# Optimization experiments

Hardware: AMD Instinct MI355X
Metric: run time of the kernel (lower is better)

## Reference

```python
import jax, jax.numpy as jnp
import numpy as np
from jax import lax

HEADS = 8
PS = 4  # window size


def setup_inputs() -> dict:
    key = jax.random.key(0)
    k1, k2, k3, k4 = jax.random.split(key, 4)
    b, c, h, w = 8, 256, 128, 128
    x = jax.random.normal(k1, (b, c, h, w), dtype=jnp.float32)
    W_qkv = jax.random.normal(k2, (3 * c, c), dtype=jnp.float32) * 0.05
    W_dw = jax.random.normal(k3, (3 * c, 1, 3, 3), dtype=jnp.float32) * 0.1
    temperature = jnp.ones((HEADS, 1, 1), dtype=jnp.float32)
    W_proj = jax.random.normal(k4, (c, c), dtype=jnp.float32) * 0.05
    return {"x": x, "W_qkv": W_qkv, "W_dw": W_dw, "temperature": temperature, "W_proj": W_proj}


def _l2norm(t, eps=1e-12):
    # matches torch F.normalize(dim=-1): x / max(||x||_2, eps)
    n = jnp.sqrt(jnp.sum(t * t, axis=-1, keepdims=True))
    return t / jnp.maximum(n, eps)


def reference(x, W_qkv, W_dw, temperature, W_proj):
    b, c, h0, w0 = x.shape
    ps, heads = PS, HEADS
    pad_h = (ps - h0 % ps) % ps
    pad_w = (ps - w0 % ps) % ps
    if pad_h or pad_w:
        x = jnp.pad(x, ((0, 0), (0, 0), (0, pad_h), (0, pad_w)))
    H, W = x.shape[2], x.shape[3]
    nh, nw = H // ps, W // ps
    d = c // heads

    # 1x1 conv -> depthwise 3x3 conv (groups = 3c, padding 1)
    qkv = jnp.einsum('oc,bchw->bohw', W_qkv, x)
    qkv = lax.conv_general_dilated(qkv, W_dw, (1, 1), 'SAME',
                                   feature_group_count=3 * c,
                                   dimension_numbers=('NCHW', 'OIHW', 'NCHW'))
    q, k, v = jnp.split(qkv, 3, axis=1)

    def win(t):
        # b (head d) (nh ps) (nw ps) -> b (nh nw) head d (ps ps)
        t = t.reshape(b, heads, d, nh, ps, nw, ps)
        t = t.transpose(0, 3, 5, 1, 2, 4, 6)  # b nh nw head d ps ps
        return t.reshape(b, nh * nw, heads, d, ps * ps)

    q, k, v = win(q), win(k), win(v)
    q = _l2norm(q)
    k = _l2norm(k)

    # channel attention over head-dim d, keys/queries live in the ps*ps window
    attn = jnp.einsum('bnhde,bnhfe->bnhdf', q, k) * temperature  # (b,n,head,d,d)
    attn = jax.nn.softmax(attn, axis=-1)
    out = jnp.einsum('bnhdf,bnhfe->bnhde', attn, v)  # (b,n,head,d,ps*ps)

    # inverse rearrange -> b (head d) H W
    out = out.reshape(b, nh, nw, heads, d, ps, ps)
    out = out.transpose(0, 3, 4, 1, 5, 2, 6).reshape(b, c, H, W)
    out = jnp.einsum('oc,bchw->bohw', W_proj, out)
    if pad_h or pad_w:
        out = out[:, :, :h0, :w0]
    return out
```

## Files before the change

kernel.cpp:

```cpp
#include <hip/hip_runtime.h>
#include <math.h>


#define HW_ (128*128)
#define CHW_ (256*128*128)

typedef __attribute__((ext_vector_type(8))) short short8;
typedef __attribute__((ext_vector_type(4))) short shortv4;
typedef __attribute__((ext_vector_type(4))) float f32x4;

static __device__ __forceinline__ unsigned short f2bf(float f) {
    unsigned int u = __float_as_uint(f);
    unsigned int r = (u + 0x7fffu + ((u >> 16) & 1u)) >> 16;
    return (unsigned short)r;
}
static __device__ __forceinline__ float bf2f(unsigned short u) {
    return __uint_as_float(((unsigned int)u) << 16);
}

__global__ __launch_bounds__(256) void conv_w(
    const float* __restrict__ Wq, const float* __restrict__ Wp,
    unsigned short* __restrict__ out)
{
    int i = blockIdx.x * 256 + threadIdx.x;
    float v = (i < 196608) ? Wq[i] : Wp[i - 196608];
    out[i] = f2bf(v);
}

__global__ __launch_bounds__(256) void gemm_qkv(
    const unsigned short* __restrict__ A,
    const float* __restrict__ x,
    unsigned short* __restrict__ qkv)
{
    __shared__ __align__(16) char smem[16896];
    shortv4* Bq = (shortv4*)(smem + 8192);

    const int t = threadIdx.x;
    const int lane = t & 63, wid = t >> 6;
    const int m0 = blockIdx.x * 128;
    const int by = blockIdx.y;
    const int nb = by >> 7;
    const int nloc0 = (by & 127) * 128;
    const int wr = wid >> 1, wc = wid & 1;
    const int l15 = lane & 15, l4 = lane >> 4;

    const unsigned short* srcA[2];
    #pragma unroll
    for (int i = 0; i < 2; ++i) {
        int u = i * 256 + t;
        int r = u >> 2, cs = u & 3;
        int c = cs ^ ((r ^ (r >> 2)) & 3);
        srcA[i] = A + (size_t)(m0 + r) * 256 + c * 8;
    }
    int ar[4];
    #pragma unroll
    for (int i = 0; i < 4; ++i) {
        int rm = wr * 64 + i * 16 + l15;
        ar[i] = rm * 4 + (l4 ^ ((rm ^ (rm >> 2)) & 3));
    }

    const int tp = t & 127, th = t >> 7;
    const float* xb = x + (size_t)nb * CHW_ + nloc0 + tp;

    f32x4 acc[4][4];
    #pragma unroll
    for (int i = 0; i < 4; ++i)
        #pragma unroll
        for (int j = 0; j < 4; ++j)
            acc[i][j] = (f32x4){0.f, 0.f, 0.f, 0.f};

    const short8* Ab = (const short8*)smem;

    for (int k0 = 0; k0 < 256; k0 += 32) {
        __syncthreads();
        float bv[16];
        #pragma unroll
        for (int j = 0; j < 4; ++j)
            #pragma unroll
            for (int i = 0; i < 4; ++i)
                bv[j * 4 + i] = xb[(size_t)(k0 + th * 16 + j * 4 + i) * HW_];
        #pragma unroll
        for (int i = 0; i < 2; ++i)
            __builtin_amdgcn_global_load_lds(
                (const __attribute__((address_space(1))) void*)(srcA[i] + k0),
                (__attribute__((address_space(3))) void*)(smem + i * 4096 + wid * 1024),
                16, 0, 0);
        #pragma unroll
        for (int j = 0; j < 4; ++j) {
            shortv4 s;
            s.x = (short)f2bf(bv[j * 4 + 0]);
            s.y = (short)f2bf(bv[j * 4 + 1]);
            s.z = (short)f2bf(bv[j * 4 + 2]);
            s.w = (short)f2bf(bv[j * 4 + 3]);
            Bq[(th * 4 + j) * 128 + tp] = s;
        }
        __syncthreads();

        short8 af[4], bf[4];
        #pragma unroll
        for (int i = 0; i < 4; ++i) {
            af[i] = Ab[ar[i]];
            int rn = wc * 64 + i * 16 + l15;
            shortv4 lo = Bq[(l4 * 2) * 128 + rn];
            shortv4 hi = Bq[(l4 * 2 + 1) * 128 + rn];
            short8 b;
            b[0] = lo.x; b[1] = lo.y; b[2] = lo.z; b[3] = lo.w;
            b[4] = hi.x; b[5] = hi.y; b[6] = hi.z; b[7] = hi.w;
            bf[i] = b;
        }
        #pragma unroll
        for (int am = 0; am < 4; ++am)
            #pragma unroll
            for (int bn = 0; bn < 4; ++bn)
                acc[am][bn] = __builtin_amdgcn_mfma_f32_16x16x32_bf16(
                    af[am], bf[bn], acc[am][bn], 0, 0, 0);
    }

    unsigned short* Co = qkv + (size_t)nb * (768 * (size_t)HW_) + nloc0;
    float* ep = (float*)smem;
    const int rr = t >> 3, c0 = (t & 7) * 16;
    #pragma unroll
    for (int am = 0; am < 4; ++am) {
        __syncthreads();
        #pragma unroll
        for (int q = 0; q < 4; ++q)
            #pragma unroll
            for (int bn = 0; bn < 4; ++bn)
                ep[(wr * 16 + l4 * 4 + q) * 132 + wc * 64 + bn * 16 + l15] =
                    acc[am][bn][q];
        __syncthreads();
        short8 o0, o1;
        #pragma unroll
        for (int j = 0; j < 8; ++j) {
            o0[j] = (short)f2bf(ep[rr * 132 + c0 + j]);
            o1[j] = (short)f2bf(ep[rr * 132 + c0 + 8 + j]);
        }
        int m = m0 + (rr >> 4) * 64 + am * 16 + (rr & 15);
        unsigned short* p = Co + (size_t)m * 16384 + c0;
        *reinterpret_cast<short8*>(p) = o0;
        *reinterpret_cast<short8*>(p + 8) = o1;
    }
}

template<int BF16OUT>
__global__ __launch_bounds__(256) void gemm_bf16(
    const unsigned short* __restrict__ A,
    const unsigned short* __restrict__ Bt,
    void* __restrict__ Cv,
    size_t strideBatch)
{
    __shared__ __align__(16) char smem[BF16OUT ? 16896 : 16384];

    const int t = threadIdx.x;
    const int lane = t & 63, wid = t >> 6;
    const int m0 = blockIdx.y * 128, n0 = blockIdx.x * 128;
    const int nb = n0 >> 14, nloc0 = n0 & 16383;
    const int wr = wid >> 1, wc = wid & 1;
    const int l15 = lane & 15, l4 = lane >> 4;

    const unsigned short* srcA[2];
    const unsigned short* srcB[2];
    #pragma unroll
    for (int i = 0; i < 2; ++i) {
        int u = i * 256 + t;
        int r = u >> 2, cs = u & 3;
        int c = cs ^ ((r ^ (r >> 2)) & 3);
        srcA[i] = A  + (size_t)(m0 + r) * 256 + c * 8;
        srcB[i] = Bt + (size_t)(n0 + r) * 256 + c * 8;
    }

    int ar[4], br[4];
    #pragma unroll
    for (int i = 0; i < 4; ++i) {
        int rm = wr * 64 + i * 16 + l15;
        ar[i] = rm * 4 + (l4 ^ ((rm ^ (rm >> 2)) & 3));
        int rn = wc * 64 + i * 16 + l15;
        br[i] = rn * 4 + (l4 ^ ((rn ^ (rn >> 2)) & 3));
    }

    f32x4 acc[4][4];
    #pragma unroll
    for (int i = 0; i < 4; ++i)
        #pragma unroll
        for (int j = 0; j < 4; ++j)
            acc[i][j] = (f32x4){0.f, 0.f, 0.f, 0.f};

    const short8* Ab = (const short8*)smem;
    const short8* Bb = (const short8*)(smem + 8192);

    for (int k0 = 0; k0 < 256; k0 += 32) {
        __syncthreads();
        #pragma unroll
        for (int i = 0; i < 2; ++i) {
            __builtin_amdgcn_global_load_lds(
                (const __attribute__((address_space(1))) void*)(srcA[i] + k0),
                (__attribute__((address_space(3))) void*)(smem + i * 4096 + wid * 1024),
                16, 0, 0);
            __builtin_amdgcn_global_load_lds(
                (const __attribute__((address_space(1))) void*)(srcB[i] + k0),
                (__attribute__((address_space(3))) void*)(smem + 8192 + i * 4096 + wid * 1024),
                16, 0, 0);
        }
        __syncthreads();
        short8 af[4], bf[4];
        #pragma unroll
        for (int i = 0; i < 4; ++i) { af[i] = Ab[ar[i]]; bf[i] = Bb[br[i]]; }
        #pragma unroll
        for (int am = 0; am < 4; ++am)
            #pragma unroll
            for (int bn = 0; bn < 4; ++bn)
                acc[am][bn] = __builtin_amdgcn_mfma_f32_16x16x32_bf16(
                    af[am], bf[bn], acc[am][bn], 0, 0, 0);
    }

    if (BF16OUT) {
        unsigned short* Co = (unsigned short*)Cv + (size_t)nb * strideBatch + nloc0;
        float* ep = (float*)smem;
        const int rr = t >> 3, c0 = (t & 7) * 16;
        #pragma unroll
        for (int am = 0; am < 4; ++am) {
            __syncthreads();
            #pragma unroll
            for (int q = 0; q < 4; ++q)
                #pragma unroll
                for (int bn = 0; bn < 4; ++bn)
                    ep[(wr * 16 + l4 * 4 + q) * 132 + wc * 64 + bn * 16 + l15] =
                        acc[am][bn][q];
            __syncthreads();
            short8 o0, o1;
            #pragma unroll
            for (int j = 0; j < 8; ++j) {
                o0[j] = (short)f2bf(ep[rr * 132 + c0 + j]);
                o1[j] = (short)f2bf(ep[rr * 132 + c0 + 8 + j]);
            }
            int m = m0 + (rr >> 4) * 64 + am * 16 + (rr & 15);
            unsigned short* p = Co + (size_t)m * 16384 + c0;
            *reinterpret_cast<short8*>(p) = o0;
            *reinterpret_cast<short8*>(p + 8) = o1;
        }
    } else {
        float* Co = (float*)Cv + (size_t)nb * strideBatch + nloc0;
        #pragma unroll
        for (int am = 0; am < 4; ++am)
            #pragma unroll
            for (int q = 0; q < 4; ++q) {
                int m = m0 + wr * 64 + am * 16 + l4 * 4 + q;
                #pragma unroll
                for (int bn = 0; bn < 4; ++bn)
                    Co[(size_t)m * 16384 + wc * 64 + bn * 16 + l15] =
                        acc[am][bn][q];
            }
    }
}

__global__ __launch_bounds__(256) void dwconv_win(
    const unsigned short* __restrict__ qkv,
    const float* __restrict__ Wdw,
    unsigned short* __restrict__ dww)
{
    const int t    = threadIdx.x;
    const int lane = t & 63;
    const int iw   = t & 31;
    const int chl  = t >> 5;
    const int wyl  = blockIdx.x;
    const int ch   = blockIdx.y * 8 + chl;
    const int bz   = blockIdx.z;

    float w[9];
    #pragma unroll
    for (int i = 0; i < 9; ++i) w[i] = Wdw[ch * 9 + i];

    float h[6][6];
    const unsigned short* plane = qkv + (size_t)(bz * 768 + ch) * HW_;
    #pragma unroll
    for (int r = 0; r < 6; ++r) {
        int gy = wyl * 4 - 1 + r;
        float c0 = 0.f, c1 = 0.f, c2 = 0.f, c3 = 0.f;
        if (gy >= 0 && gy < 128) {
            ushort4 u = *reinterpret_cast<const ushort4*>(
                plane + (size_t)gy * 128 + iw * 4);
            c0 = bf2f(u.x); c1 = bf2f(u.y); c2 = bf2f(u.z); c3 = bf2f(u.w);
        }
        float lf = __shfl(c3, (lane + 63) & 63);
        float rt = __shfl(c0, (lane + 1) & 63);
        h[r][0] = (iw == 0)  ? 0.f : lf;
        h[r][1] = c0; h[r][2] = c1; h[r][3] = c2; h[r][4] = c3;
        h[r][5] = (iw == 31) ? 0.f : rt;
    }

    unsigned short* outp =
        dww + ((size_t)(bz * 1024 + wyl * 32 + iw) * 768 + ch) * 16;
    short8 o0, o1;
    #pragma unroll
    for (int py = 0; py < 4; ++py) {
        #pragma unroll
        for (int px = 0; px < 4; ++px) {
            float s = 0.f;
            #pragma unroll
            for (int dy = 0; dy < 3; ++dy)
                #pragma unroll
                for (int dx = 0; dx < 3; ++dx)
                    s += h[py + dy][px + dx] * w[dy * 3 + dx];
            int e = py * 4 + px;
            if (e < 8) o0[e] = (short)f2bf(s); else o1[e - 8] = (short)f2bf(s);
        }
    }
    *reinterpret_cast<short8*>(outp) = o0;
    *reinterpret_cast<short8*>(outp + 8) = o1;
}

__global__ __launch_bounds__(256) void attn2(
    const unsigned short* __restrict__ dww,
    const float* __restrict__ temp,
    unsigned short* __restrict__ attnT)
{
    __shared__ float kv[512 * 20];
    const int t   = threadIdx.x;
    const int iw  = blockIdx.x;
    const int wyl = blockIdx.y;
    const int bz  = blockIdx.z;
    const int win = bz * 1024 + wyl * 32 + iw;
    const unsigned short* src = dww + (size_t)win * 12288;

    float q[16], kr[16], vr[16];
    {
        short8 a0 = *reinterpret_cast<const short8*>(src + t * 16);
        short8 a1 = *reinterpret_cast<const short8*>(src + t * 16 + 8);
        short8 b0 = *reinterpret_cast<const short8*>(src + (256 + t) * 16);
        short8 b1 = *reinterpret_cast<const short8*>(src + (256 + t) * 16 + 8);
        short8 c0 = *reinterpret_cast<const short8*>(src + (512 + t) * 16);
        short8 c1 = *reinterpret_cast<const short8*>(src + (512 + t) * 16 + 8);
        #pragma unroll
        for (int j = 0; j < 8; ++j) {
            q[j]      = bf2f((unsigned short)a0[j]);
            q[8 + j]  = bf2f((unsigned short)a1[j]);
            kr[j]     = bf2f((unsigned short)b0[j]);
            kr[8 + j] = bf2f((unsigned short)b1[j]);
            vr[j]     = bf2f((unsigned short)c0[j]);
            vr[8 + j] = bf2f((unsigned short)c1[j]);
        }
    }

    {
        float sq = 0.f, sk = 0.f;
        #pragma unroll
        for (int e = 0; e < 16; ++e) { sq += q[e] * q[e]; sk += kr[e] * kr[e]; }
        float cq = 1.0f / fmaxf(sqrtf(sq), 1e-12f);
        float ck = 1.0f / fmaxf(sqrtf(sk), 1e-12f);
        #pragma unroll
        for (int e = 0; e < 16; ++e) { q[e] *= cq; kr[e] *= ck; }
    }

    {
        float* kp = &kv[t * 20];
        float* vp = &kv[(256 + t) * 20];
        #pragma unroll
        for (int j = 0; j < 4; ++j) {
            *reinterpret_cast<float4*>(kp + j * 4) =
                make_float4(kr[j*4], kr[j*4+1], kr[j*4+2], kr[j*4+3]);
            *reinterpret_cast<float4*>(vp + j * 4) =
                make_float4(vr[j*4], vr[j*4+1], vr[j*4+2], vr[j*4+3]);
        }
    }
    __syncthreads();

    const int head = t >> 5;
    const float tmpv = temp[head];
    const float* kb = &kv[(head * 32) * 20];
    const float* vb = &kv[(256 + head * 32) * 20];

    float lg[32];
    float mx = -1e30f;
    #pragma unroll
    for (int f = 0; f < 32; ++f) {
        float s = 0.f;
        #pragma unroll
        for (int j = 0; j < 4; ++j) {
            float4 k4 = *reinterpret_cast<const float4*>(kb + f * 20 + j * 4);
            s += q[j*4] * k4.x + q[j*4+1] * k4.y + q[j*4+2] * k4.z + q[j*4+3] * k4.w;
        }
        s *= tmpv;
        lg[f] = s;
        mx = fmaxf(mx, s);
    }
    float sum = 0.f;
    #pragma unroll
    for (int f = 0; f < 32; ++f) { lg[f] = __expf(lg[f] - mx); sum += lg[f]; }
    const float inv = 1.0f / sum;

    float o[16];
    #pragma unroll
    for (int e = 0; e < 16; ++e) o[e] = 0.f;
    #pragma unroll
    for (int f = 0; f < 32; ++f) {
        float p = lg[f];
        #pragma unroll
        for (int j = 0; j < 4; ++j) {
            float4 v4 = *reinterpret_cast<const float4*>(vb + f * 20 + j * 4);
            o[j*4]   += p * v4.x; o[j*4+1] += p * v4.y;
            o[j*4+2] += p * v4.z; o[j*4+3] += p * v4.w;
        }
    }

    #pragma unroll
    for (int e = 0; e < 16; ++e) {
        int py = e >> 2, px = e & 3;
        size_t pl = (size_t)bz * HW_ + (wyl * 4 + py) * 128 + iw * 4 + px;
        attnT[pl * 256 + t] = f2bf(o[e] * inv);
    }
}

extern "C" void kernel_launch(void* const* d_in, const int* in_sizes, int n_in,
                              void* d_out, int out_size, void* d_ws, size_t ws_size,
                              hipStream_t stream) {
    const float* x     = (const float*)d_in[0];
    const float* Wqkv  = (const float*)d_in[1];
    const float* Wdw   = (const float*)d_in[2];
    const float* temp  = (const float*)d_in[3];
    const float* Wproj = (const float*)d_in[4];
    float* out = (float*)d_out;

    unsigned short* Wb = (unsigned short*)d_ws;
    const size_t offW = 262144 * 2;

    const size_t qkvB = (size_t)768 * HW_ * 2;
    const size_t dwwB = (size_t)1024 * 768 * 16 * 2;
    const size_t atB  = (size_t)HW_ * 256 * 2;
    const size_t perB = qkvB + dwwB + atB;

    int G = 4;
    while (G > 1 && offW + (size_t)G * perB > ws_size) G >>= 1;

    unsigned short* qkv   = (unsigned short*)((char*)d_ws + offW);
    unsigned short* dww   = (unsigned short*)((char*)d_ws + offW + (size_t)G * qkvB);
    unsigned short* attnT = (unsigned short*)((char*)d_ws + offW + (size_t)G * (qkvB + dwwB));

    conv_w<<<1024, 256, 0, stream>>>(Wqkv, Wproj, Wb);

    for (int b0 = 0; b0 < 8; b0 += G) {
        gemm_qkv<<<dim3(6, G * 128), 256, 0, stream>>>(
            Wb, x + (size_t)b0 * CHW_, qkv);

        dwconv_win<<<dim3(32, 96, G), 256, 0, stream>>>(
            qkv, Wdw, dww);

        attn2<<<dim3(32, 32, G), 256, 0, stream>>>(
            dww, temp, attnT);

        gemm_bf16<0><<<dim3(G * 128, 2), 256, 0, stream>>>(
            Wb + 196608, attnT, out + (size_t)b0 * CHW_, (size_t)CHW_);
    }
}
```

Baseline: 410.3 us.

## Vectorize x loads in QKV GEMM, swap proj grid order, raise batch group

The QKV GEMM now loads x with float4 reads (four pixels per thread across four channels) and packs the bf16 values into a new padded LDS layout with 16-byte stores, replacing scalar loads and 8-byte stores. The projection GEMM grid is transposed so the two M-blocks sharing one N-tile are adjacent, which improves L2 reuse of the attention tile, and its unused bf16 epilogue is removed. The batch group size G is raised from 4 to 8 when the workspace allows it, which means fewer launches and larger grids but needs more workspace memory.

```diff
diff --git a/kernel.cpp b/kernel.cpp
--- a/kernel.cpp
+++ b/kernel.cpp
@@ -33,8 +33,6 @@
     unsigned short* __restrict__ qkv)
 {
     __shared__ __align__(16) char smem[16896];
-    shortv4* Bq = (shortv4*)(smem + 8192);
-
     const int t = threadIdx.x;
     const int lane = t & 63, wid = t >> 6;
     const int m0 = blockIdx.x * 128;
@@ -59,8 +57,11 @@
         ar[i] = rm * 4 + (l4 ^ ((rm ^ (rm >> 2)) & 3));
     }
 
-    const int tp = t & 127, th = t >> 7;
-    const float* xb = x + (size_t)nb * CHW_ + nloc0 + tp;
+    const int pl  = (t & 31) * 4;
+    const int chq = t >> 5;
+    const float* xb = x + (size_t)nb * CHW_ + nloc0 + pl;
+    char* Bbase = smem + 8192;
+    char* bwp = Bbase + chq * 1056 + pl * 8;
 
     f32x4 acc[4][4];
     #pragma unroll
@@ -73,27 +74,38 @@
 
     for (int k0 = 0; k0 < 256; k0 += 32) {
         __syncthreads();
-        float bv[16];
-        #pragma unroll
-        for (int j = 0; j < 4; ++j)
-            #pragma unroll
-            for (int i = 0; i < 4; ++i)
-                bv[j * 4 + i] = xb[(size_t)(k0 + th * 16 + j * 4 + i) * HW_];
         #pragma unroll
         for (int i = 0; i < 2; ++i)
             __builtin_amdgcn_global_load_lds(
                 (const __attribute__((address_space(1))) void*)(srcA[i] + k0),
                 (__attribute__((address_space(3))) void*)(smem + i * 4096 + wid * 1024),
                 16, 0, 0);
-        #pragma unroll
-        for (int j = 0; j < 4; ++j) {
-            shortv4 s;
-            s.x = (short)f2bf(bv[j * 4 + 0]);
-            s.y = (short)f2bf(bv[j * 4 + 1]);
-            s.z = (short)f2bf(bv[j * 4 + 2]);
-            s.w = (short)f2bf(bv[j * 4 + 3]);
-            Bq[(th * 4 + j) * 128 + tp] = s;
-        }
+        float4 vx[4];
+        #pragma unroll
+        for (int j = 0; j < 4; ++j)
+            vx[j] = *reinterpret_cast<const float4*>(
+                xb + (size_t)(k0 + chq * 4 + j) * HW_);
+        short8 w0, w1;
+        #pragma unroll
+        for (int p = 0; p < 4; ++p) {
+            const float* f0 = (const float*)&vx[0];
+            const float* f1 = (const float*)&vx[1];
+            const float* f2 = (const float*)&vx[2];
+            const float* f3 = (const float*)&vx[3];
+            short v0 = (short)f2bf(f0[p]);
+            short v1 = (short)f2bf(f1[p]);
+            short v2 = (short)f2bf(f2[p]);
+            short v3 = (short)f2bf(f3[p]);
+            if (p < 2) {
+                w0[p * 4 + 0] = v0; w0[p * 4 + 1] = v1;
+                w0[p * 4 + 2] = v2; w0[p * 4 + 3] = v3;
+            } else {
+                w1[(p - 2) * 4 + 0] = v0; w1[(p - 2) * 4 + 1] = v1;
+                w1[(p - 2) * 4 + 2] = v2; w1[(p - 2) * 4 + 3] = v3;
+            }
+        }
+        *reinterpret_cast<short8*>(bwp)      = w0;
+        *reinterpret_cast<short8*>(bwp + 16) = w1;
         __syncthreads();
 
         short8 af[4], bf[4];
@@ -101,8 +113,10 @@
         for (int i = 0; i < 4; ++i) {
             af[i] = Ab[ar[i]];
             int rn = wc * 64 + i * 16 + l15;
-            shortv4 lo = Bq[(l4 * 2) * 128 + rn];
-            shortv4 hi = Bq[(l4 * 2 + 1) * 128 + rn];
+            shortv4 lo = *reinterpret_cast<const shortv4*>(
+                Bbase + (l4 * 2) * 1056 + rn * 8);
+            shortv4 hi = *reinterpret_cast<const shortv4*>(
+                Bbase + (l4 * 2 + 1) * 1056 + rn * 8);
             short8 b;
             b[0] = lo.x; b[1] = lo.y; b[2] = lo.z; b[3] = lo.w;
             b[4] = hi.x; b[5] = hi.y; b[6] = hi.z; b[7] = hi.w;
@@ -149,11 +163,12 @@
     void* __restrict__ Cv,
     size_t strideBatch)
 {
-    __shared__ __align__(16) char smem[BF16OUT ? 16896 : 16384];
+    __shared__ __align__(16) char smem[16384];
 
     const int t = threadIdx.x;
     const int lane = t & 63, wid = t >> 6;
-    const int m0 = blockIdx.y * 128, n0 = blockIdx.x * 128;
+    const int m0 = blockIdx.x * 128;
+    const int n0 = blockIdx.y * 128;
     const int nb = n0 >> 14, nloc0 = n0 & 16383;
     const int wr = wid >> 1, wc = wid & 1;
     const int l15 = lane & 15, l4 = lane >> 4;
@@ -213,44 +228,17 @@
                     af[am], bf[bn], acc[am][bn], 0, 0, 0);
     }
 
-    if (BF16OUT) {
-        unsigned short* Co = (unsigned short*)Cv + (size_t)nb * strideBatch + nloc0;
-        float* ep = (float*)smem;
-        const int rr = t >> 3, c0 = (t & 7) * 16;
-        #pragma unroll
-        for (int am = 0; am < 4; ++am) {
-            __syncthreads();
+    float* Co = (float*)Cv + (size_t)nb * strideBatch + nloc0;
+    #pragma unroll
+    for (int am = 0; am < 4; ++am)
+        #pragma unroll
+        for (int q = 0; q < 4; ++q) {
+            int m = m0 + wr * 64 + am * 16 + l4 * 4 + q;
             #pragma unroll
-            for (int q = 0; q < 4; ++q)
-                #pragma unroll
-                for (int bn = 0; bn < 4; ++bn)
-                    ep[(wr * 16 + l4 * 4 + q) * 132 + wc * 64 + bn * 16 + l15] =
-                        acc[am][bn][q];
-            __syncthreads();
-            short8 o0, o1;
-            #pragma unroll
-            for (int j = 0; j < 8; ++j) {
-                o0[j] = (short)f2bf(ep[rr * 132 + c0 + j]);
-                o1[j] = (short)f2bf(ep[rr * 132 + c0 + 8 + j]);
-            }
-            int m = m0 + (rr >> 4) * 64 + am * 16 + (rr & 15);
-            unsigned short* p = Co + (size_t)m * 16384 + c0;
-            *reinterpret_cast<short8*>(p) = o0;
-            *reinterpret_cast<short8*>(p + 8) = o1;
-        }
-    } else {
-        float* Co = (float*)Cv + (size_t)nb * strideBatch + nloc0;
-        #pragma unroll
-        for (int am = 0; am < 4; ++am)
-            #pragma unroll
-            for (int q = 0; q < 4; ++q) {
-                int m = m0 + wr * 64 + am * 16 + l4 * 4 + q;
-                #pragma unroll
-                for (int bn = 0; bn < 4; ++bn)
-                    Co[(size_t)m * 16384 + wc * 64 + bn * 16 + l15] =
-                        acc[am][bn][q];
-            }
-    }
+            for (int bn = 0; bn < 4; ++bn)
+                Co[(size_t)m * 16384 + wc * 64 + bn * 16 + l15] =
+                    acc[am][bn][q];
+        }
 }
 
 __global__ __launch_bounds__(256) void dwconv_win(
@@ -428,7 +416,7 @@
     const size_t atB  = (size_t)HW_ * 256 * 2;
     const size_t perB = qkvB + dwwB + atB;
 
-    int G = 4;
+    int G = 8;
     while (G > 1 && offW + (size_t)G * perB > ws_size) G >>= 1;
 
     unsigned short* qkv   = (unsigned short*)((char*)d_ws + offW);
@@ -447,7 +435,7 @@
         attn2<<<dim3(32, 32, G), 256, 0, stream>>>(
             dww, temp, attnT);
 
-        gemm_bf16<0><<<dim3(G * 128, 2), 256, 0, stream>>>(
+        gemm_bf16<0><<<dim3(2, G * 128), 256, 0, stream>>>(
             Wb + 196608, attnT, out + (size_t)b0 * CHW_, (size_t)CHW_);
     }
 }
```

Result: no change. 411.1 us (+0.2%).
